# Performance work log

Hardware: AMD Instinct MI355X
Metric: run time of the kernel (lower is better)

Reference implementation:

```python
import jax, jax.numpy as jnp
import numpy as np

# Dimensions (all layers are mLSTM due to the constructor bug: `if w` tests the
# whole truthy `which` list, so signature=(2,1) still yields 3 mLSTM layers).
L, S, B, I = 3, 512, 4, 512      # layers, seq_len, batch, inp_dim
H, D = 8, 64                     # head_num, head_dim
HD = H * D                       # hidden dim = 512
P = 2 * I                        # up_l projection dim (m-branch p_factor = 2)
K = 4                            # causal conv kernel size
EPS = 1e-5
PNAMES = ['ln_g', 'ln_b', 'upl_w', 'upl_b', 'upr_w', 'upr_b', 'conv_w', 'conv_b',
          'wq_w', 'wq_b', 'wk_w', 'wk_b', 'wv_w', 'wv_b', 'wo_w', 'wo_b',
          'wi_w', 'wi_b', 'wf_w', 'wf_b', 'skip_w', 'gn_g', 'gn_b', 'down_w', 'down_b']


def setup_inputs() -> dict:
    key = jax.random.key(0)
    ks = iter(jax.random.split(key, 16))
    def w(shape, fan_in):
        return jax.random.normal(next(ks), shape, jnp.float32) / np.float32(np.sqrt(fan_in))
    return {
        'seq': jax.random.normal(next(ks), (S, B, I), jnp.float32),
        'ln_g': jnp.ones((L, I), jnp.float32), 'ln_b': jnp.zeros((L, I), jnp.float32),
        'upl_w': w((L, P, I), I), 'upl_b': jnp.zeros((L, P), jnp.float32),
        'upr_w': w((L, HD, I), I), 'upr_b': jnp.zeros((L, HD), jnp.float32),
        'conv_w': w((L, K), K), 'conv_b': jnp.zeros((L,), jnp.float32),
        'wq_w': w((L, HD, P), P), 'wq_b': jnp.zeros((L, HD), jnp.float32),
        'wk_w': w((L, HD, P), P), 'wk_b': jnp.zeros((L, HD), jnp.float32),
        'wv_w': w((L, HD, P), P), 'wv_b': jnp.zeros((L, HD), jnp.float32),
        'wo_w': w((L, HD, P), P), 'wo_b': jnp.zeros((L, HD), jnp.float32),
        'wi_w': w((L, H, P), P), 'wi_b': jnp.zeros((L, H), jnp.float32),
        'wf_w': w((L, H, P), P), 'wf_b': jnp.zeros((L, H), jnp.float32),
        'skip_w': w((L, HD, P), P),
        'gn_g': jnp.ones((L, HD), jnp.float32), 'gn_b': jnp.zeros((L, HD), jnp.float32),
        'down_w': w((L, I, HD), HD), 'down_b': jnp.zeros((L, I), jnp.float32),
    }


def _layernorm(x, g, b):
    mu = x.mean(-1, keepdims=True)
    v = ((x - mu) ** 2).mean(-1, keepdims=True)
    return (x - mu) / jnp.sqrt(v + EPS) * g + b


def _groupnorm(x, g, b):
    # GroupNorm(head_num, HD) on (B, HD): normalize each head's D channels
    xh = x.reshape(-1, H, D)
    mu = xh.mean(-1, keepdims=True)
    v = ((xh - mu) ** 2).mean(-1, keepdims=True)
    xn = (xh - mu) / jnp.sqrt(v + EPS)
    return (xn * g.reshape(H, D) + b.reshape(H, D)).reshape(-1, HD)


def _causal_conv(x, w, b):
    # 1-channel causal conv over the feature axis of the per-step vector (B, P)
    xp = jnp.pad(x, ((0, 0), (K - 1, 0)))
    y = b
    for k in range(K):  # K=4, static unroll
        y = y + w[k] * xp[:, k:k + x.shape[1]]
    return y


def _mlstm_step(p, x, state):
    c_, n_, m_ = state
    x_n = _layernorm(x, p['ln_g'], p['ln_b'])
    x_t = x_n @ p['upl_w'].T + p['upl_b']                 # (B, P)
    r_t = x_n @ p['upr_w'].T + p['upr_b']                 # (B, HD)
    x_c = jax.nn.silu(_causal_conv(x_t, p['conv_w'], p['conv_b']))
    q = (x_c @ p['wq_w'].T + p['wq_b']).reshape(-1, H, D)
    k = (x_c @ p['wk_w'].T + p['wk_b']).reshape(-1, H, D) / np.float32(np.sqrt(D))
    v = (x_t @ p['wv_w'].T + p['wv_b']).reshape(-1, H, D)
    i = x_c @ p['wi_w'].T + p['wi_b']                     # (B, H)
    f = x_c @ p['wf_w'].T + p['wf_b']                     # (B, H)
    o = jax.nn.sigmoid(x_t @ p['wo_w'].T + p['wo_b'])     # (B, HD)
    m = jnp.maximum(f + m_, i)                            # stabilizer
    ig = jnp.exp(i - m)
    fg = jnp.exp(f - m + m_)
    c = fg[..., None, None] * c_ + ig[..., None, None] * jnp.einsum('bhd,bhe->bhde', v, k)
    n = fg[..., None] * n_ + ig[..., None] * k
    num = jnp.einsum('bhde,bhe->bhd', c, q)
    den = jnp.maximum(jnp.abs(jnp.einsum('bhd,bhd->bh', n, q)), 1.0)[..., None]
    h = o * (num / den).reshape(-1, HD)
    out = _groupnorm(h, p['gn_g'], p['gn_b']) + x_c @ p['skip_w'].T
    out = out * jax.nn.silu(r_t)
    out = out @ p['down_w'].T + p['down_b']
    return out + x, (c, n, m)


def _forward(seq, params):
    b = seq.shape[1]
    def step(states, x_t):
        new_states = []
        inp = x_t
        for l in range(L):
            pl = {k: v[l] for k, v in params.items()}
            inp, st = _mlstm_step(pl, inp, states[l])
            new_states.append(st)
        return tuple(new_states), inp
    init = tuple((jnp.zeros((b, H, D, D), seq.dtype),
                  jnp.ones((b, H, D), seq.dtype),
                  jnp.zeros((b, H), seq.dtype)) for _ in range(L))
    _, out = jax.lax.scan(step, init, seq)
    return out  # (S, B, I)


def reference(seq, ln_g, ln_b, upl_w, upl_b, upr_w, upr_b, conv_w, conv_b,
              wq_w, wq_b, wk_w, wk_b, wv_w, wv_b, wo_w, wo_b,
              wi_w, wi_b, wf_w, wf_b, skip_w, gn_g, gn_b, down_w, down_b):
    params = dict(zip(PNAMES, [ln_g, ln_b, upl_w, upl_b, upr_w, upr_b, conv_w, conv_b,
                               wq_w, wq_b, wk_w, wk_b, wv_w, wv_b, wo_w, wo_b,
                               wi_w, wi_b, wf_w, wf_b, skip_w, gn_g, gn_b, down_w, down_b]))
    return _forward(seq, params)
```

## Files before the change

kernel.cpp:

```cpp
#include <hip/hip_runtime.h>
#include <hip/hip_bf16.h>
#include <cstdint>
#include <cstddef>

typedef short short8 __attribute__((ext_vector_type(8)));
typedef short short4v __attribute__((ext_vector_type(4)));
typedef float f32x4 __attribute__((ext_vector_type(4)));
typedef __hip_bfloat16 bf16;

#define NROW 2048
#define N1 1536
#define N2 1664
#define N3 1024
#define EPSV 1e-5f

static __device__ __forceinline__ bf16 f2bf(float v){ return __float2bfloat16(v); }
static __device__ __forceinline__ float bfbits2f(short s){
  unsigned u = ((unsigned)(unsigned short)s) << 16;
  float f; __builtin_memcpy(&f, &u, 4); return f;
}
static __device__ __forceinline__ void split_bf(float v, bf16& h, bf16& l){
  h = __float2bfloat16(v);
  l = __float2bfloat16(v - __bfloat162float(h));
}

static __device__ __forceinline__ void gload16(const bf16* g, bf16* l){
  __builtin_amdgcn_global_load_lds(
      (const __attribute__((address_space(1))) void*)(g),
      (__attribute__((address_space(3))) void*)(l), 16, 0, 0);
}

#define MFMA __builtin_amdgcn_mfma_f32_16x16x32_bf16

__global__ __launch_bounds__(256) void pack_w1(const float* __restrict__ upl,
    const float* __restrict__ upr, bf16* __restrict__ dh, bf16* __restrict__ dl)
{
  int l = blockIdx.y, r = blockIdx.x;
  const float* src = (r < 1024) ? upl + ((size_t)l*1024 + r)*512
                                : upr + ((size_t)l*512 + (r-1024))*512;
  size_t o = ((size_t)l*N1 + r)*512;
  for (int c = threadIdx.x; c < 512; c += 256) split_bf(src[c], dh[o+c], dl[o+c]);
}

__global__ __launch_bounds__(256) void pack_w2(const float* __restrict__ wq,
    const float* __restrict__ wk, const float* __restrict__ skp,
    const float* __restrict__ wi, const float* __restrict__ wf,
    bf16* __restrict__ dh, bf16* __restrict__ dl)
{
  int l = blockIdx.y, r = blockIdx.x;
  const float* src; float sc = 1.f;
  if (r < 512)        src = wq  + ((size_t)l*512 + r)*1024;
  else if (r < 1024){ src = wk  + ((size_t)l*512 + r-512)*1024; sc = 0.125f; }
  else if (r < 1536)  src = skp + ((size_t)l*512 + r-1024)*1024;
  else if (r < 1544)  src = wi  + ((size_t)l*8   + r-1536)*1024;
  else if (r < 1552)  src = wf  + ((size_t)l*8   + r-1544)*1024;
  else src = nullptr;
  size_t o = ((size_t)l*N2 + r)*1024;
  for (int c = threadIdx.x; c < 1024; c += 256)
    split_bf(src ? src[c]*sc : 0.f, dh[o+c], dl[o+c]);
}

__global__ __launch_bounds__(256) void pack_w3(const float* __restrict__ wv,
    const float* __restrict__ wo, bf16* __restrict__ dh, bf16* __restrict__ dl)
{
  int l = blockIdx.y, r = blockIdx.x;
  const float* src = (r < 512) ? wv + ((size_t)l*512 + r)*1024
                               : wo + ((size_t)l*512 + (r-512))*1024;
  size_t o = ((size_t)l*N3 + r)*1024;
  for (int c = threadIdx.x; c < 1024; c += 256) split_bf(src[c], dh[o+c], dl[o+c]);
}

__global__ __launch_bounds__(256) void pack_w4(const float* __restrict__ dw,
    bf16* __restrict__ dh, bf16* __restrict__ dl)
{
  int l = blockIdx.y, r = blockIdx.x;
  const float* src = dw + ((size_t)l*512 + r)*512;
  size_t o = ((size_t)l*512 + r)*512;
  for (int c = threadIdx.x; c < 512; c += 256) split_bf(src[c], dh[o+c], dl[o+c]);
}

__global__ __launch_bounds__(256) void pack_bias(
    const float* __restrict__ uplb, const float* __restrict__ uprb,
    const float* __restrict__ wqb,  const float* __restrict__ wkb,
    const float* __restrict__ wib,  const float* __restrict__ wfb,
    const float* __restrict__ wvb,  const float* __restrict__ wob,
    const float* __restrict__ dwb,
    float* __restrict__ b1, float* __restrict__ b2,
    float* __restrict__ b3, float* __restrict__ b4)
{
  int l = blockIdx.x;
  for (int j = threadIdx.x; j < N1; j += 256)
    b1[l*N1+j] = (j < 1024) ? uplb[l*1024+j] : uprb[l*512+j-1024];
  for (int j = threadIdx.x; j < N2; j += 256){
    float v = 0.f;
    if (j < 512)        v = wqb[l*512+j];
    else if (j < 1024)  v = wkb[l*512+j-512]*0.125f;
    else if (j < 1536)  v = 0.f;
    else if (j < 1544)  v = wib[l*8+j-1536];
    else if (j < 1552)  v = wfb[l*8+j-1544];
    b2[l*N2+j] = v;
  }
  for (int j = threadIdx.x; j < N3; j += 256)
    b3[l*N3+j] = (j < 512) ? wvb[l*512+j] : wob[l*512+j-512];
  for (int j = threadIdx.x; j < 512; j += 256)
    b4[l*512+j] = dwb[l*512+j];
}

static __device__ __forceinline__ void gemm_core(
    bf16* __restrict__ sm,
    int bx, int by,
    const bf16* __restrict__ Ah, const bf16* __restrict__ Al,
    const bf16* __restrict__ Wh, const bf16* __restrict__ Wl,
    const float* __restrict__ bias, float* __restrict__ Cf,
    bf16* __restrict__ Cbh, bf16* __restrict__ Cbl,
    const float* __restrict__ resid, int N, int K)
{
  int tid = threadIdx.x;
  int lane = tid & 63, w = tid >> 6;
  int wr = w >> 2, wc = w & 3;
  int m0 = by*128, n0 = bx*128;
  int srow = tid >> 2, sslot = tid & 3;
  int gcol = ((sslot ^ (srow & 3)) * 8);
  const bf16* gAh = Ah + (size_t)(m0 + srow)*K + gcol;
  const bf16* gAl = Al + (size_t)(m0 + srow)*K + gcol;
  const bf16* gBh = Wh + (size_t)(n0 + srow)*K + gcol;
  const bf16* gBl = Wl + (size_t)(n0 + srow)*K + gcol;

  f32x4 acc[4][2];
  for (int i=0;i<4;i++) for (int j=0;j<2;j++) acc[i][j] = (f32x4){0.f,0.f,0.f,0.f};

  int r = lane & 15, g = lane >> 4;
  int xs = (g ^ (r & 3)) * 8;
  int aoff[4], boff[2];
  for (int mi=0;mi<4;mi++) aoff[mi] = (wr*64 + mi*16 + r)*32 + xs;
  for (int ni=0;ni<2;ni++) boff[ni] = (wc*32 + ni*16 + r)*32 + xs;

  int nt = K >> 5;
#define STAGE_T(base, kk) do{ bf16* _d = sm + (base) + tid*8; \
    gload16(gAh + (kk), _d); \
    gload16(gAl + (kk), _d + 4096); \
    gload16(gBh + (kk), _d + 8192); \
    gload16(gBl + (kk), _d + 12288); }while(0)

  STAGE_T(0, 0);
  asm volatile("s_waitcnt vmcnt(0)" ::: "memory");
  __builtin_amdgcn_s_barrier();

  for (int t = 0; t < nt; ++t){
    int cb = (t & 1) * 16384;
    if (t + 1 < nt) STAGE_T(16384 - cb, (t+1)*32);
    const bf16* sA = sm + cb;
    short8 ah[4], al[4], bh2[2], bl2[2];
    for (int mi=0;mi<4;mi++){
      ah[mi] = *(const short8*)(sA + aoff[mi]);
      al[mi] = *(const short8*)(sA + 4096 + aoff[mi]);
    }
    for (int ni=0;ni<2;ni++){
      bh2[ni] = *(const short8*)(sA + 8192 + boff[ni]);
      bl2[ni] = *(const short8*)(sA + 12288 + boff[ni]);
    }
    for (int mi=0;mi<4;mi++) for (int ni=0;ni<2;ni++)
      acc[mi][ni] = MFMA(ah[mi], bh2[ni], acc[mi][ni],0,0,0);
    for (int mi=0;mi<4;mi++) for (int ni=0;ni<2;ni++)
      acc[mi][ni] = MFMA(al[mi], bh2[ni], acc[mi][ni],0,0,0);
    for (int mi=0;mi<4;mi++) for (int ni=0;ni<2;ni++)
      acc[mi][ni] = MFMA(ah[mi], bl2[ni], acc[mi][ni],0,0,0);
    asm volatile("s_waitcnt vmcnt(0)" ::: "memory");
    __builtin_amdgcn_s_barrier();
  }
#undef STAGE_T

  for (int mi=0;mi<4;mi++) for (int ni=0;ni<2;ni++){
    int col = n0 + wc*32 + ni*16 + r;
    float bv = bias ? bias[col] : 0.f;
    for (int j=0;j<4;j++){
      int row = m0 + wr*64 + mi*16 + g*4 + j;
      float v = acc[mi][ni][j] + bv;
      size_t o = (size_t)row*N + col;
      if (resid) v += resid[o];
      if (Cf) Cf[o] = v;
      if (Cbh) split_bf(v, Cbh[o], Cbl[o]);
    }
  }
}

__global__ __launch_bounds__(512) void gemm_std(
    const bf16* __restrict__ Ah, const bf16* __restrict__ Al,
    const bf16* __restrict__ Wh, const bf16* __restrict__ Wl,
    const float* __restrict__ bias, float* __restrict__ Cf,
    bf16* __restrict__ Cbh, bf16* __restrict__ Cbl,
    const float* __restrict__ resid, int N, int K, int nbx)
{
  __shared__ bf16 sm[2*4*4096];
  int id = blockIdx.x;
  int cpx = gridDim.x >> 3;
  int swz = (id & 7)*cpx + (id >> 3);
  int by = swz / nbx, bx = swz - by*nbx;
  gemm_core(sm, bx, by, Ah, Al, Wh, Wl, bias, Cf, Cbh, Cbl, resid, N, K);
}

__global__ __launch_bounds__(512) void gemm23(
    const bf16* __restrict__ A2h, const bf16* __restrict__ A2l,
    const bf16* __restrict__ W2h, const bf16* __restrict__ W2l,
    const float* __restrict__ b2,
    bf16* __restrict__ c2h, bf16* __restrict__ c2l,
    const bf16* __restrict__ A3h, const bf16* __restrict__ A3l,
    const bf16* __restrict__ W3h, const bf16* __restrict__ W3l,
    const float* __restrict__ b3,
    bf16* __restrict__ c3h, bf16* __restrict__ c3l)
{
  __shared__ bf16 sm[2*4*4096];
  int id = blockIdx.x;
  int cpx = gridDim.x >> 3;
  int swz = (id & 7)*cpx + (id >> 3);
  int by = swz / 21, bx = swz - by*21;
  if (bx < 13)
    gemm_core(sm, bx, by, A2h, A2l, W2h, W2l, b2, nullptr, c2h, c2l, nullptr, N2, 1024);
  else
    gemm_core(sm, bx-13, by, A3h, A3l, W3h, W3l, b3, nullptr, c3h, c3l, nullptr, N3, 1024);
}

__global__ __launch_bounds__(256) void ln_kernel(const float* __restrict__ x,
    const float* __restrict__ g, const float* __restrict__ bt,
    bf16* __restrict__ xnh, bf16* __restrict__ xnl)
{
  int row = blockIdx.x, t = threadIdx.x;
  float v0 = x[(size_t)row*512 + t], v1 = x[(size_t)row*512 + 256 + t];
  float s = v0 + v1, ss = v0*v0 + v1*v1;
  for (int m=1; m<64; m<<=1){ s += __shfl_xor(s,m); ss += __shfl_xor(ss,m); }
  __shared__ float sh[8];
  int w = t >> 6, lane = t & 63;
  if (lane == 0){ sh[w] = s; sh[4+w] = ss; }
  __syncthreads();
  s = sh[0]+sh[1]+sh[2]+sh[3]; ss = sh[4]+sh[5]+sh[6]+sh[7];
  float mu = s*(1.f/512.f), var = ss*(1.f/512.f) - mu*mu;
  float rs = rsqrtf(var + EPSV);
  float y0 = (v0-mu)*rs*g[t]     + bt[t];
  float y1 = (v1-mu)*rs*g[256+t] + bt[256+t];
  split_bf(y0, xnh[(size_t)row*512 + t],       xnl[(size_t)row*512 + t]);
  split_bf(y1, xnh[(size_t)row*512 + 256 + t], xnl[(size_t)row*512 + 256 + t]);
}

__global__ __launch_bounds__(256) void conv_kernel(
    const bf16* __restrict__ c1h, const bf16* __restrict__ c1l,
    const float* __restrict__ cw, const float* __restrict__ cb,
    bf16* __restrict__ xch, bf16* __restrict__ xcl,
    bf16* __restrict__ xth, bf16* __restrict__ xtl)
{
  int row = blockIdx.x;
  size_t rb = (size_t)row*N1;
  float w0=cw[0], w1=cw[1], w2=cw[2], w3=cw[3], bb=cb[0];
  int j0 = threadIdx.x*4;
  float x[7];
  for (int k=0;k<3;k++){
    int j = j0-3+k;
    x[k] = (j>=0) ? (bfbits2f(*(const short*)(c1h+rb+j)) +
                     bfbits2f(*(const short*)(c1l+rb+j))) : 0.f;
  }
  short4v h4 = *(const short4v*)(c1h+rb+j0);
  short4v l4 = *(const short4v*)(c1l+rb+j0);
  for (int k=0;k<4;k++) x[3+k] = bfbits2f(h4[k]) + bfbits2f(l4[k]);
  for (int i=0;i<4;i++){
    float y = bb + w0*x[i] + w1*x[i+1] + w2*x[i+2] + w3*x[i+3];
    float sg = 1.f/(1.f + __expf(-y));
    size_t o = (size_t)row*1024 + j0 + i;
    split_bf(y*sg, xch[o], xcl[o]);
    split_bf(x[3+i], xth[o], xtl[o]);
  }
}

__global__ __launch_bounds__(512) void scan_kernel(
    const bf16* __restrict__ c2h, const bf16* __restrict__ c2l,
    float* __restrict__ rowterm, float* __restrict__ colterm,
    float* __restrict__ den0)
{
  int bh = blockIdx.x, b = bh >> 3, h = bh & 7;
  int t = threadIdx.x;
  size_t rowoff = (size_t)(t*4+b)*N2;
  float fv = bfbits2f(*(const short*)(c2h+rowoff+1544+h)) +
             bfbits2f(*(const short*)(c2l+rowoff+1544+h));
  float iv = bfbits2f(*(const short*)(c2h+rowoff+1536+h)) +
             bfbits2f(*(const short*)(c2l+rowoff+1536+h));
  __shared__ double a[512];
  a[t] = (double)fv; __syncthreads();
  for (int off=1; off<512; off<<=1){
    double x = a[t];
    double y = (t >= off) ? a[t-off] : 0.0;
    __syncthreads();
    a[t] = x + y;
    __syncthreads();
  }
  float ct = (float)((double)iv - a[t]);
  colterm[bh*512 + t] = ct;
  __shared__ float mx[512];
  mx[t] = ct; __syncthreads();
  for (int off=1; off<512; off<<=1){
    float x = mx[t];
    float y = (t >= off) ? mx[t-off] : -3.0e38f;
    __syncthreads();
    mx[t] = fmaxf(x, y);
    __syncthreads();
  }
  float rt = -fmaxf(0.f, mx[t]);
  rowterm[bh*512 + t] = rt;
  float qs = 0.f;
  size_t qoff = rowoff + h*64;
  for (int c8=0;c8<8;c8++){
    short8 hx = *(const short8*)(c2h+qoff+c8*8);
    short8 lx = *(const short8*)(c2l+qoff+c8*8);
    for (int e=0;e<8;e++) qs += bfbits2f(hx[e]) + bfbits2f(lx[e]);
  }
  den0[bh*512 + t] = __expf(rt) * qs;
}

__global__ __launch_bounds__(512) void vtrans_kernel(
    const bf16* __restrict__ c3h, const bf16* __restrict__ c3l,
    bf16* __restrict__ vTh, bf16* __restrict__ vTl)
{
  int bh = blockIdx.y, b = bh >> 3, h = bh & 7;
  int d0 = blockIdx.x*8;
  int s = threadIdx.x;
  for (int dd=0; dd<8; dd++){
    int d = d0 + dd;
    size_t i = (size_t)(s*4+b)*N3 + h*64 + d;
    size_t o = ((size_t)bh*64 + d)*512 + s;
    vTh[o] = c3h[i];
    vTl[o] = c3l[i];
  }
}

__global__ __launch_bounds__(256) void attn_kernel(
    const bf16* __restrict__ c2h, const bf16* __restrict__ c2l,
    const bf16* __restrict__ vTh, const bf16* __restrict__ vTl,
    const float* __restrict__ rowt, const float* __restrict__ colt,
    float* __restrict__ num, float* __restrict__ denp)
{
  __shared__ bf16 Ph[32*64], Pl[32*64];
  int lane = threadIdx.x & 63, w = threadIdx.x >> 6;
  int tb = blockIdx.x, bh = blockIdx.y, b = bh >> 3, h = bh & 7;
  int t0 = tb*32;
  int r = lane & 15, g = lane >> 4;
  int rq = g*4;

  short8 qh[2][2], ql[2][2];
  for (int mi=0;mi<2;mi++) for (int k0=0;k0<2;k0++){
    size_t off = (size_t)((t0+mi*16+r)*4+b)*N2 + h*64 + k0*32 + g*8;
    qh[mi][k0] = *(const short8*)(c2h+off);
    ql[mi][k0] = *(const short8*)(c2l+off);
  }
  const float* rt = rowt + bh*512;
  const float* ctm = colt + bh*512;
  float rtv[2][4];
  for (int mi=0;mi<2;mi++) for (int j=0;j<4;j++) rtv[mi][j] = rt[t0+mi*16+rq+j];

  f32x4 accPV[2];
  for (int i=0;i<2;i++) accPV[i] = (f32x4){0.f,0.f,0.f,0.f};
  float rsum[2][4];
  for (int i=0;i<2;i++) for (int j=0;j<4;j++) rsum[i][j] = 0.f;

  int nsb = (tb >> 1) + 1;
  for (int sb=0; sb<nsb; ++sb){
    int s0 = sb*64;
    f32x4 acc[2];
    for (int i=0;i<2;i++) acc[i] = (f32x4){0.f,0.f,0.f,0.f};
    short8 kh[2], kl[2];
    for (int k0=0;k0<2;k0++){
      size_t off = (size_t)((s0+w*16+r)*4+b)*N2 + 512 + h*64 + k0*32 + g*8;
      kh[k0] = *(const short8*)(c2h+off);
      kl[k0] = *(const short8*)(c2l+off);
    }
    for (int k0=0;k0<2;k0++){
      for (int mi=0;mi<2;mi++) acc[mi] = MFMA(qh[mi][k0], kh[k0], acc[mi],0,0,0);
      for (int mi=0;mi<2;mi++) acc[mi] = MFMA(ql[mi][k0], kh[k0], acc[mi],0,0,0);
      for (int mi=0;mi<2;mi++) acc[mi] = MFMA(qh[mi][k0], kl[k0], acc[mi],0,0,0);
    }
    int sl = w*16 + r;
    int s = s0 + sl;
    float ctv = ctm[s];
    for (int mi=0;mi<2;mi++){
      for (int j=0;j<4;j++){
        int tloc = mi*16 + rq + j;
        int t = t0 + tloc;
        float wg = (s <= t) ? __expf(rtv[mi][j] + ctv) : 0.f;
        float gv = acc[mi][j] * wg;
        rsum[mi][j] += gv;
        int col = ((((sl>>3) ^ (tloc&7))<<3) | (sl&7));
        split_bf(gv, Ph[tloc*64+col], Pl[tloc*64+col]);
      }
    }
    __syncthreads();
    short8 vh[2], vl[2];
    for (int k0=0;k0<2;k0++){
      size_t off = ((size_t)bh*64 + w*16 + r)*512 + s0 + k0*32 + g*8;
      vh[k0] = *(const short8*)(vTh+off);
      vl[k0] = *(const short8*)(vTl+off);
    }
    for (int k0=0;k0<2;k0++){
      short8 ph[2], pl[2];
      for (int mi=0;mi<2;mi++){
        int tloc = mi*16 + r;
        int slot = (k0*4 + g) ^ (tloc&7);
        ph[mi] = *(const short8*)(&Ph[tloc*64 + slot*8]);
        pl[mi] = *(const short8*)(&Pl[tloc*64 + slot*8]);
      }
      for (int mi=0;mi<2;mi++) accPV[mi] = MFMA(ph[mi], vh[k0], accPV[mi],0,0,0);
      for (int mi=0;mi<2;mi++) accPV[mi] = MFMA(pl[mi], vh[k0], accPV[mi],0,0,0);
      for (int mi=0;mi<2;mi++) accPV[mi] = MFMA(ph[mi], vl[k0], accPV[mi],0,0,0);
    }
    __syncthreads();
  }

  for (int mi=0;mi<2;mi++)
    for (int j=0;j<4;j++){
      int t = t0 + mi*16 + rq + j;
      num[((size_t)bh*512 + t)*64 + w*16 + r] = accPV[mi][j];
    }
  for (int mi=0;mi<2;mi++)
    for (int j=0;j<4;j++){
      float v = rsum[mi][j];
      v += __shfl_xor(v,1); v += __shfl_xor(v,2);
      v += __shfl_xor(v,4); v += __shfl_xor(v,8);
      if (r == 0){
        int t = t0 + mi*16 + rq + j;
        denp[((size_t)bh*512 + t)*4 + w] = v;
      }
    }
}

__global__ __launch_bounds__(512) void h_kernel(
    const float* __restrict__ num, const float* __restrict__ den0,
    const float* __restrict__ denp,
    const bf16* __restrict__ c2h, const bf16* __restrict__ c2l,
    const bf16* __restrict__ c3h, const bf16* __restrict__ c3l,
    const bf16* __restrict__ c1h, const bf16* __restrict__ c1l,
    const float* __restrict__ gng, const float* __restrict__ gnb,
    bf16* __restrict__ oph, bf16* __restrict__ opl)
{
  int row = blockIdx.x, t = row >> 2, b = row & 3;
  int h = threadIdx.x >> 6, d = threadIdx.x & 63;
  int bh = b*8 + h;
  size_t bt = (size_t)bh*512 + t;
  float dn = den0[bt];
  for (int p=0; p<4; p++) dn += denp[bt*4 + p];
  dn = fmaxf(fabsf(dn), 1.f);
  float nv = num[bt*64 + d];
  size_t io = (size_t)row*N3 + 512 + h*64 + d;
  float ov = bfbits2f(*(const short*)(c3h+io)) + bfbits2f(*(const short*)(c3l+io));
  float o = 1.f/(1.f + __expf(-ov));
  float hv = o * nv / dn;
  float s = hv, ss = hv*hv;
  for (int m=1; m<64; m<<=1){ s += __shfl_xor(s,m); ss += __shfl_xor(ss,m); }
  float mu = s*(1.f/64.f), var = ss*(1.f/64.f) - mu*mu;
  float gn = (hv - mu)*rsqrtf(var + EPSV)*gng[h*64+d] + gnb[h*64+d];
  size_t ks = (size_t)row*N2 + 1024 + h*64 + d;
  float sk = bfbits2f(*(const short*)(c2h+ks)) + bfbits2f(*(const short*)(c2l+ks));
  size_t kr = (size_t)row*N1 + 1024 + h*64 + d;
  float rv = bfbits2f(*(const short*)(c1h+kr)) + bfbits2f(*(const short*)(c1l+kr));
  float y = (gn + sk) * (rv/(1.f + __expf(-rv)));
  size_t oo = (size_t)row*512 + h*64 + d;
  split_bf(y, oph[oo], opl[oo]);
}

extern "C" void kernel_launch(void* const* d_in, const int* in_sizes, int n_in,
                              void* d_out, int out_size, void* d_ws, size_t ws_size,
                              hipStream_t stream)
{
  (void)in_sizes; (void)n_in; (void)out_size; (void)ws_size;
  const float* seq    = (const float*)d_in[0];
  const float* ln_g   = (const float*)d_in[1];
  const float* ln_b   = (const float*)d_in[2];
  const float* upl_w  = (const float*)d_in[3];
  const float* upl_b  = (const float*)d_in[4];
  const float* upr_w  = (const float*)d_in[5];
  const float* upr_b  = (const float*)d_in[6];
  const float* conv_w = (const float*)d_in[7];
  const float* conv_b = (const float*)d_in[8];
  const float* wq_w   = (const float*)d_in[9];
  const float* wq_b   = (const float*)d_in[10];
  const float* wk_w   = (const float*)d_in[11];
  const float* wk_b   = (const float*)d_in[12];
  const float* wv_w   = (const float*)d_in[13];
  const float* wv_b   = (const float*)d_in[14];
  const float* wo_w   = (const float*)d_in[15];
  const float* wo_b   = (const float*)d_in[16];
  const float* wi_w   = (const float*)d_in[17];
  const float* wi_b   = (const float*)d_in[18];
  const float* wf_w   = (const float*)d_in[19];
  const float* wf_b   = (const float*)d_in[20];
  const float* skip_w = (const float*)d_in[21];
  const float* gn_g   = (const float*)d_in[22];
  const float* gn_b   = (const float*)d_in[23];
  const float* down_w = (const float*)d_in[24];
  const float* down_b = (const float*)d_in[25];

  char* ws = (char*)d_ws;
  size_t off = 0;
  auto alloc = [&](size_t bytes)->char*{
    char* p = ws + off; off = (off + bytes + 255) & ~(size_t)255; return p;
  };
  bf16*  W1h = (bf16*)alloc((size_t)3*N1*512*2);
  bf16*  W1l = (bf16*)alloc((size_t)3*N1*512*2);
  bf16*  W2h = (bf16*)alloc((size_t)3*N2*1024*2);
  bf16*  W2l = (bf16*)alloc((size_t)3*N2*1024*2);
  bf16*  W3h = (bf16*)alloc((size_t)3*N3*1024*2);
  bf16*  W3l = (bf16*)alloc((size_t)3*N3*1024*2);
  bf16*  W4h = (bf16*)alloc((size_t)3*512*512*2);
  bf16*  W4l = (bf16*)alloc((size_t)3*512*512*2);
  float* b1  = (float*)alloc((size_t)3*N1*4);
  float* b2  = (float*)alloc((size_t)3*N2*4);
  float* b3  = (float*)alloc((size_t)3*N3*4);
  float* b4  = (float*)alloc((size_t)3*512*4);
  bf16*  xnh = (bf16*)alloc((size_t)NROW*512*2);
  bf16*  xnl = (bf16*)alloc((size_t)NROW*512*2);
  bf16*  c1h = (bf16*)alloc((size_t)NROW*N1*2);
  bf16*  c1l = (bf16*)alloc((size_t)NROW*N1*2);
  bf16*  xth = (bf16*)alloc((size_t)NROW*1024*2);
  bf16*  xtl = (bf16*)alloc((size_t)NROW*1024*2);
  bf16*  xch = (bf16*)alloc((size_t)NROW*1024*2);
  bf16*  xcl = (bf16*)alloc((size_t)NROW*1024*2);
  bf16*  c2h = (bf16*)alloc((size_t)NROW*N2*2);
  bf16*  c2l = (bf16*)alloc((size_t)NROW*N2*2);
  bf16*  c3h = (bf16*)alloc((size_t)NROW*N3*2);
  bf16*  c3l = (bf16*)alloc((size_t)NROW*N3*2);
  bf16*  vTh = (bf16*)alloc((size_t)32*64*512*2);
  bf16*  vTl = (bf16*)alloc((size_t)32*64*512*2);
  float* rowt= (float*)alloc((size_t)32*512*4);
  float* colt= (float*)alloc((size_t)32*512*4);
  float* den0= (float*)alloc((size_t)32*512*4);
  float* denp= (float*)alloc((size_t)32*512*4*4);
  float* num = (float*)alloc((size_t)32*512*64*4);
  bf16*  oph = (bf16*)alloc((size_t)NROW*512*2);
  bf16*  opl = (bf16*)alloc((size_t)NROW*512*2);
  float* xA  = (float*)alloc((size_t)NROW*512*4);
  float* xB  = (float*)alloc((size_t)NROW*512*4);

  pack_w1<<<dim3(N1,3), 256, 0, stream>>>(upl_w, upr_w, W1h, W1l);
  pack_w2<<<dim3(N2,3), 256, 0, stream>>>(wq_w, wk_w, skip_w, wi_w, wf_w, W2h, W2l);
  pack_w3<<<dim3(N3,3), 256, 0, stream>>>(wv_w, wo_w, W3h, W3l);
  pack_w4<<<dim3(512,3), 256, 0, stream>>>(down_w, W4h, W4l);
  pack_bias<<<3, 256, 0, stream>>>(upl_b, upr_b, wq_b, wk_b, wi_b, wf_b,
                                   wv_b, wo_b, down_b, b1, b2, b3, b4);

  for (int l = 0; l < 3; l++){
    const float* x_in = (l == 0) ? seq : ((l == 1) ? xA : xB);
    float* x_out = (l == 0) ? xA : ((l == 1) ? xB : (float*)d_out);

    ln_kernel<<<NROW, 256, 0, stream>>>(x_in, ln_g + l*512, ln_b + l*512, xnh, xnl);
    gemm_std<<<12*16, 512, 0, stream>>>(
        xnh, xnl, W1h + (size_t)l*N1*512, W1l + (size_t)l*N1*512,
        b1 + l*N1, nullptr, c1h, c1l, nullptr, N1, 512, 12);
    conv_kernel<<<NROW, 256, 0, stream>>>(c1h, c1l, conv_w + l*4, conv_b + l,
                                          xch, xcl, xth, xtl);
    gemm23<<<21*16, 512, 0, stream>>>(
        xch, xcl, W2h + (size_t)l*N2*1024, W2l + (size_t)l*N2*1024, b2 + l*N2,
        c2h, c2l,
        xth, xtl, W3h + (size_t)l*N3*1024, W3l + (size_t)l*N3*1024, b3 + l*N3,
        c3h, c3l);
    scan_kernel<<<32, 512, 0, stream>>>(c2h, c2l, rowt, colt, den0);
    vtrans_kernel<<<dim3(8,32), 512, 0, stream>>>(c3h, c3l, vTh, vTl);
    attn_kernel<<<dim3(16,32), 256, 0, stream>>>(c2h, c2l, vTh, vTl,
                                                 rowt, colt, num, denp);
    h_kernel<<<NROW, 512, 0, stream>>>(num, den0, denp, c2h, c2l, c3h, c3l,
                                       c1h, c1l, gn_g + l*512, gn_b + l*512,
                                       oph, opl);
    gemm_std<<<4*16, 512, 0, stream>>>(
        oph, opl, W4h + (size_t)l*512*512, W4l + (size_t)l*512*512,
        b4 + l*512, x_out, nullptr, nullptr, x_in, 512, 512, 4);
  }
}
```

Before: 459.8 us.

## Merge pack and prep kernels, use 64-row GEMM tiles, warp-level scans

Merges the four weight-pack kernels and the bias pack into one launch, and merges the gate scan with the V transpose into a single prep kernel. The scan now runs in one wavefront using register prefix sums and shuffles instead of a 512-thread LDS scan with many barriers. The q-sum denominator term moves into h_kernel. The up-projection and down-projection GEMMs switch to a 64x128-tile, 256-thread variant so more blocks fill the device. The aim is to cut launch count, barrier latency and under-occupancy of the small GEMMs, at the cost of less weight reuse per tile.

Measured after the change: 410.0 us. 10.8% less time.

```diff
diff --git a/kernel.cpp b/kernel.cpp
--- a/kernel.cpp
+++ b/kernel.cpp
@@ -32,78 +32,72 @@
 
 #define MFMA __builtin_amdgcn_mfma_f32_16x16x32_bf16
 
-__global__ __launch_bounds__(256) void pack_w1(const float* __restrict__ upl,
-    const float* __restrict__ upr, bf16* __restrict__ dh, bf16* __restrict__ dl)
-{
-  int l = blockIdx.y, r = blockIdx.x;
-  const float* src = (r < 1024) ? upl + ((size_t)l*1024 + r)*512
-                                : upr + ((size_t)l*512 + (r-1024))*512;
-  size_t o = ((size_t)l*N1 + r)*512;
-  for (int c = threadIdx.x; c < 512; c += 256) split_bf(src[c], dh[o+c], dl[o+c]);
-}
-
-__global__ __launch_bounds__(256) void pack_w2(const float* __restrict__ wq,
-    const float* __restrict__ wk, const float* __restrict__ skp,
-    const float* __restrict__ wi, const float* __restrict__ wf,
-    bf16* __restrict__ dh, bf16* __restrict__ dl)
-{
-  int l = blockIdx.y, r = blockIdx.x;
-  const float* src; float sc = 1.f;
-  if (r < 512)        src = wq  + ((size_t)l*512 + r)*1024;
-  else if (r < 1024){ src = wk  + ((size_t)l*512 + r-512)*1024; sc = 0.125f; }
-  else if (r < 1536)  src = skp + ((size_t)l*512 + r-1024)*1024;
-  else if (r < 1544)  src = wi  + ((size_t)l*8   + r-1536)*1024;
-  else if (r < 1552)  src = wf  + ((size_t)l*8   + r-1544)*1024;
-  else src = nullptr;
-  size_t o = ((size_t)l*N2 + r)*1024;
-  for (int c = threadIdx.x; c < 1024; c += 256)
-    split_bf(src ? src[c]*sc : 0.f, dh[o+c], dl[o+c]);
-}
-
-__global__ __launch_bounds__(256) void pack_w3(const float* __restrict__ wv,
-    const float* __restrict__ wo, bf16* __restrict__ dh, bf16* __restrict__ dl)
-{
-  int l = blockIdx.y, r = blockIdx.x;
-  const float* src = (r < 512) ? wv + ((size_t)l*512 + r)*1024
-                               : wo + ((size_t)l*512 + (r-512))*1024;
-  size_t o = ((size_t)l*N3 + r)*1024;
-  for (int c = threadIdx.x; c < 1024; c += 256) split_bf(src[c], dh[o+c], dl[o+c]);
-}
-
-__global__ __launch_bounds__(256) void pack_w4(const float* __restrict__ dw,
-    bf16* __restrict__ dh, bf16* __restrict__ dl)
-{
-  int l = blockIdx.y, r = blockIdx.x;
-  const float* src = dw + ((size_t)l*512 + r)*512;
-  size_t o = ((size_t)l*512 + r)*512;
-  for (int c = threadIdx.x; c < 512; c += 256) split_bf(src[c], dh[o+c], dl[o+c]);
-}
-
-__global__ __launch_bounds__(256) void pack_bias(
+__global__ __launch_bounds__(256) void pack_all(
+    const float* __restrict__ upl, const float* __restrict__ upr,
+    const float* __restrict__ wq,  const float* __restrict__ wk,
+    const float* __restrict__ skp, const float* __restrict__ wi,
+    const float* __restrict__ wf,  const float* __restrict__ wv,
+    const float* __restrict__ wo,  const float* __restrict__ dw,
     const float* __restrict__ uplb, const float* __restrict__ uprb,
     const float* __restrict__ wqb,  const float* __restrict__ wkb,
     const float* __restrict__ wib,  const float* __restrict__ wfb,
     const float* __restrict__ wvb,  const float* __restrict__ wob,
     const float* __restrict__ dwb,
+    bf16* __restrict__ W1h, bf16* __restrict__ W1l,
+    bf16* __restrict__ W2h, bf16* __restrict__ W2l,
+    bf16* __restrict__ W3h, bf16* __restrict__ W3l,
+    bf16* __restrict__ W4h, bf16* __restrict__ W4l,
     float* __restrict__ b1, float* __restrict__ b2,
     float* __restrict__ b3, float* __restrict__ b4)
 {
-  int l = blockIdx.x;
-  for (int j = threadIdx.x; j < N1; j += 256)
-    b1[l*N1+j] = (j < 1024) ? uplb[l*1024+j] : uprb[l*512+j-1024];
-  for (int j = threadIdx.x; j < N2; j += 256){
-    float v = 0.f;
-    if (j < 512)        v = wqb[l*512+j];
-    else if (j < 1024)  v = wkb[l*512+j-512]*0.125f;
-    else if (j < 1536)  v = 0.f;
-    else if (j < 1544)  v = wib[l*8+j-1536];
-    else if (j < 1552)  v = wfb[l*8+j-1544];
-    b2[l*N2+j] = v;
-  }
-  for (int j = threadIdx.x; j < N3; j += 256)
-    b3[l*N3+j] = (j < 512) ? wvb[l*512+j] : wob[l*512+j-512];
-  for (int j = threadIdx.x; j < 512; j += 256)
-    b4[l*512+j] = dwb[l*512+j];
+  int l = blockIdx.y;
+  int bx = blockIdx.x;
+  if (bx < 1536){
+    int r = bx;
+    const float* src = (r < 1024) ? upl + ((size_t)l*1024 + r)*512
+                                  : upr + ((size_t)l*512 + (r-1024))*512;
+    size_t o = ((size_t)l*N1 + r)*512;
+    for (int c = threadIdx.x; c < 512; c += 256) split_bf(src[c], W1h[o+c], W1l[o+c]);
+  } else if (bx < 3200){
+    int r = bx - 1536;
+    const float* src; float sc = 1.f;
+    if (r < 512)        src = wq  + ((size_t)l*512 + r)*1024;
+    else if (r < 1024){ src = wk  + ((size_t)l*512 + r-512)*1024; sc = 0.125f; }
+    else if (r < 1536)  src = skp + ((size_t)l*512 + r-1024)*1024;
+    else if (r < 1544)  src = wi  + ((size_t)l*8   + r-1536)*1024;
+    else if (r < 1552)  src = wf  + ((size_t)l*8   + r-1544)*1024;
+    else src = nullptr;
+    size_t o = ((size_t)l*N2 + r)*1024;
+    for (int c = threadIdx.x; c < 1024; c += 256)
+      split_bf(src ? src[c]*sc : 0.f, W2h[o+c], W2l[o+c]);
+  } else if (bx < 4224){
+    int r = bx - 3200;
+    const float* src = (r < 512) ? wv + ((size_t)l*512 + r)*1024
+                                 : wo + ((size_t)l*512 + (r-512))*1024;
+    size_t o = ((size_t)l*N3 + r)*1024;
+    for (int c = threadIdx.x; c < 1024; c += 256) split_bf(src[c], W3h[o+c], W3l[o+c]);
+  } else if (bx < 4736){
+    int r = bx - 4224;
+    const float* src = dw + ((size_t)l*512 + r)*512;
+    size_t o = ((size_t)l*512 + r)*512;
+    for (int c = threadIdx.x; c < 512; c += 256) split_bf(src[c], W4h[o+c], W4l[o+c]);
+  } else {
+    for (int j = threadIdx.x; j < N1; j += 256)
+      b1[l*N1+j] = (j < 1024) ? uplb[l*1024+j] : uprb[l*512+j-1024];
+    for (int j = threadIdx.x; j < N2; j += 256){
+      float v = 0.f;
+      if (j < 512)        v = wqb[l*512+j];
+      else if (j < 1024)  v = wkb[l*512+j-512]*0.125f;
+      else if (j < 1536)  v = 0.f;
+      else if (j < 1544)  v = wib[l*8+j-1536];
+      else if (j < 1552)  v = wfb[l*8+j-1544];
+      b2[l*N2+j] = v;
+    }
+    for (int j = threadIdx.x; j < N3; j += 256)
+      b3[l*N3+j] = (j < 512) ? wvb[l*512+j] : wob[l*512+j-512];
+    for (int j = threadIdx.x; j < 512; j += 256)
+      b4[l*512+j] = dwb[l*512+j];
+  }
 }
 
 static __device__ __forceinline__ void gemm_core(
@@ -184,6 +178,84 @@
   }
 }
 
+static __device__ __forceinline__ void gemm_core64(
+    bf16* __restrict__ sm,
+    int bx, int by,
+    const bf16* __restrict__ Ah, const bf16* __restrict__ Al,
+    const bf16* __restrict__ Wh, const bf16* __restrict__ Wl,
+    const float* __restrict__ bias, float* __restrict__ Cf,
+    bf16* __restrict__ Cbh, bf16* __restrict__ Cbl,
+    const float* __restrict__ resid, int N, int K)
+{
+  int tid = threadIdx.x;
+  int lane = tid & 63, w = tid >> 6;
+  int m0 = by*64, n0 = bx*128;
+  int srow = tid >> 2, sslot = tid & 3;
+  int gcol = ((sslot ^ (srow & 3)) * 8);
+  const bf16* gAh = Ah + (size_t)(m0 + srow)*K + gcol;
+  const bf16* gAl = Al + (size_t)(m0 + srow)*K + gcol;
+  const bf16* gBh = Wh + (size_t)(n0 + srow)*K + gcol;
+  const bf16* gBl = Wl + (size_t)(n0 + srow)*K + gcol;
+  size_t pstr = (size_t)64*K;
+
+  f32x4 acc[4][2];
+  for (int i=0;i<4;i++) for (int j=0;j<2;j++) acc[i][j] = (f32x4){0.f,0.f,0.f,0.f};
+
+  int r = lane & 15, g = lane >> 4;
+  int xs = (g ^ (r & 3)) * 8;
+  int aoff[4], boff[2];
+  for (int mi=0;mi<4;mi++) aoff[mi] = (mi*16 + r)*32 + xs;
+  for (int ni=0;ni<2;ni++) boff[ni] = (w*32 + ni*16 + r)*32 + xs;
+
+  int nt = K >> 5;
+#define STAGE64(base, kk) do{ bf16* _d = sm + (base) + tid*8; \
+    gload16(gAh + (kk), _d); \
+    gload16(gAl + (kk), _d + 2048); \
+    gload16(gBh + (kk), _d + 4096);  gload16(gBh + (kk) + pstr, _d + 6144); \
+    gload16(gBl + (kk), _d + 8192);  gload16(gBl + (kk) + pstr, _d + 10240); }while(0)
+
+  STAGE64(0, 0);
+  asm volatile("s_waitcnt vmcnt(0)" ::: "memory");
+  __builtin_amdgcn_s_barrier();
+
+  for (int t = 0; t < nt; ++t){
+    int cb = (t & 1) * 12288;
+    if (t + 1 < nt) STAGE64(12288 - cb, (t+1)*32);
+    const bf16* sA = sm + cb;
+    short8 ah[4], al[4], bh2[2], bl2[2];
+    for (int mi=0;mi<4;mi++){
+      ah[mi] = *(const short8*)(sA + aoff[mi]);
+      al[mi] = *(const short8*)(sA + 2048 + aoff[mi]);
+    }
+    for (int ni=0;ni<2;ni++){
+      bh2[ni] = *(const short8*)(sA + 4096 + boff[ni]);
+      bl2[ni] = *(const short8*)(sA + 8192 + boff[ni]);
+    }
+    for (int mi=0;mi<4;mi++) for (int ni=0;ni<2;ni++)
+      acc[mi][ni] = MFMA(ah[mi], bh2[ni], acc[mi][ni],0,0,0);
+    for (int mi=0;mi<4;mi++) for (int ni=0;ni<2;ni++)
+      acc[mi][ni] = MFMA(al[mi], bh2[ni], acc[mi][ni],0,0,0);
+    for (int mi=0;mi<4;mi++) for (int ni=0;ni<2;ni++)
+      acc[mi][ni] = MFMA(ah[mi], bl2[ni], acc[mi][ni],0,0,0);
+    asm volatile("s_waitcnt vmcnt(0)" ::: "memory");
+    __builtin_amdgcn_s_barrier();
+  }
+#undef STAGE64
+
+  for (int mi=0;mi<4;mi++) for (int ni=0;ni<2;ni++){
+    int col = n0 + w*32 + ni*16 + r;
+    float bv = bias ? bias[col] : 0.f;
+    for (int j=0;j<4;j++){
+      int row = m0 + mi*16 + g*4 + j;
+      float v = acc[mi][ni][j] + bv;
+      size_t o = (size_t)row*N + col;
+      if (resid) v += resid[o];
+      if (Cf) Cf[o] = v;
+      if (Cbh) split_bf(v, Cbh[o], Cbl[o]);
+    }
+  }
+}
+
 __global__ __launch_bounds__(512) void gemm_std(
     const bf16* __restrict__ Ah, const bf16* __restrict__ Al,
     const bf16* __restrict__ Wh, const bf16* __restrict__ Wl,
@@ -197,6 +269,21 @@
   int swz = (id & 7)*cpx + (id >> 3);
   int by = swz / nbx, bx = swz - by*nbx;
   gemm_core(sm, bx, by, Ah, Al, Wh, Wl, bias, Cf, Cbh, Cbl, resid, N, K);
+}
+
+__global__ __launch_bounds__(256) void gemm_s64(
+    const bf16* __restrict__ Ah, const bf16* __restrict__ Al,
+    const bf16* __restrict__ Wh, const bf16* __restrict__ Wl,
+    const float* __restrict__ bias, float* __restrict__ Cf,
+    bf16* __restrict__ Cbh, bf16* __restrict__ Cbl,
+    const float* __restrict__ resid, int N, int K, int nbx)
+{
+  __shared__ bf16 sm[2*12288];
+  int id = blockIdx.x;
+  int cpx = gridDim.x >> 3;
+  int swz = (id & 7)*cpx + (id >> 3);
+  int by = swz / nbx, bx = swz - by*nbx;
+  gemm_core64(sm, bx, by, Ah, Al, Wh, Wl, bias, Cf, Cbh, Cbl, resid, N, K);
 }
 
 __global__ __launch_bounds__(512) void gemm23(
@@ -269,63 +356,61 @@
   }
 }
 
-__global__ __launch_bounds__(512) void scan_kernel(
+__global__ __launch_bounds__(512) void prep_kernel(
+    const bf16* __restrict__ c3h, const bf16* __restrict__ c3l,
     const bf16* __restrict__ c2h, const bf16* __restrict__ c2l,
-    float* __restrict__ rowterm, float* __restrict__ colterm,
-    float* __restrict__ den0)
-{
-  int bh = blockIdx.x, b = bh >> 3, h = bh & 7;
-  int t = threadIdx.x;
-  size_t rowoff = (size_t)(t*4+b)*N2;
-  float fv = bfbits2f(*(const short*)(c2h+rowoff+1544+h)) +
-             bfbits2f(*(const short*)(c2l+rowoff+1544+h));
-  float iv = bfbits2f(*(const short*)(c2h+rowoff+1536+h)) +
-             bfbits2f(*(const short*)(c2l+rowoff+1536+h));
-  __shared__ double a[512];
-  a[t] = (double)fv; __syncthreads();
-  for (int off=1; off<512; off<<=1){
-    double x = a[t];
-    double y = (t >= off) ? a[t-off] : 0.0;
-    __syncthreads();
-    a[t] = x + y;
-    __syncthreads();
-  }
-  float ct = (float)((double)iv - a[t]);
-  colterm[bh*512 + t] = ct;
-  __shared__ float mx[512];
-  mx[t] = ct; __syncthreads();
-  for (int off=1; off<512; off<<=1){
-    float x = mx[t];
-    float y = (t >= off) ? mx[t-off] : -3.0e38f;
-    __syncthreads();
-    mx[t] = fmaxf(x, y);
-    __syncthreads();
-  }
-  float rt = -fmaxf(0.f, mx[t]);
-  rowterm[bh*512 + t] = rt;
-  float qs = 0.f;
-  size_t qoff = rowoff + h*64;
-  for (int c8=0;c8<8;c8++){
-    short8 hx = *(const short8*)(c2h+qoff+c8*8);
-    short8 lx = *(const short8*)(c2l+qoff+c8*8);
-    for (int e=0;e<8;e++) qs += bfbits2f(hx[e]) + bfbits2f(lx[e]);
-  }
-  den0[bh*512 + t] = __expf(rt) * qs;
-}
-
-__global__ __launch_bounds__(512) void vtrans_kernel(
-    const bf16* __restrict__ c3h, const bf16* __restrict__ c3l,
-    bf16* __restrict__ vTh, bf16* __restrict__ vTl)
+    bf16* __restrict__ vTh, bf16* __restrict__ vTl,
+    float* __restrict__ rowterm, float* __restrict__ colterm)
 {
   int bh = blockIdx.y, b = bh >> 3, h = bh & 7;
-  int d0 = blockIdx.x*8;
-  int s = threadIdx.x;
-  for (int dd=0; dd<8; dd++){
-    int d = d0 + dd;
-    size_t i = (size_t)(s*4+b)*N3 + h*64 + d;
-    size_t o = ((size_t)bh*64 + d)*512 + s;
-    vTh[o] = c3h[i];
-    vTl[o] = c3l[i];
+  if (blockIdx.x < 8){
+    int d0 = blockIdx.x*8;
+    int s = threadIdx.x;
+    for (int dd=0; dd<8; dd++){
+      int d = d0 + dd;
+      size_t i = (size_t)(s*4+b)*N3 + h*64 + d;
+      size_t o = ((size_t)bh*64 + d)*512 + s;
+      vTh[o] = c3h[i];
+      vTl[o] = c3l[i];
+    }
+    return;
+  }
+  if (threadIdx.x >= 64) return;
+  int lane = threadIdx.x;
+  double fv[8]; float iv[8];
+  for (int j=0;j<8;j++){
+    int t = lane*8 + j;
+    size_t ro = (size_t)(t*4+b)*N2;
+    fv[j] = (double)(bfbits2f(*(const short*)(c2h+ro+1544+h)) +
+                     bfbits2f(*(const short*)(c2l+ro+1544+h)));
+    iv[j] = bfbits2f(*(const short*)(c2h+ro+1536+h)) +
+            bfbits2f(*(const short*)(c2l+ro+1536+h));
+  }
+  double ps[8]; double s = 0.0;
+  for (int j=0;j<8;j++){ s += fv[j]; ps[j] = s; }
+  double run = s;
+  for (int o=1;o<64;o<<=1){
+    double u = __shfl_up(run, o);
+    if (lane >= o) run += u;
+  }
+  double excl = run - s;
+  float ct[8];
+  for (int j=0;j<8;j++){
+    ct[j] = (float)((double)iv[j] - (excl + ps[j]));
+    colterm[bh*512 + lane*8 + j] = ct[j];
+  }
+  float pm[8]; float mm = -3.0e38f;
+  for (int j=0;j<8;j++){ mm = fmaxf(mm, ct[j]); pm[j] = mm; }
+  float incl = mm;
+  for (int o=1;o<64;o<<=1){
+    float u = __shfl_up(incl, o);
+    if (lane >= o) incl = fmaxf(incl, u);
+  }
+  float ex = __shfl_up(incl, 1);
+  if (lane == 0) ex = -3.0e38f;
+  for (int j=0;j<8;j++){
+    float inc = fmaxf(ex, pm[j]);
+    rowterm[bh*512 + lane*8 + j] = -fmaxf(0.f, inc);
   }
 }
 
@@ -428,8 +513,8 @@
 }
 
 __global__ __launch_bounds__(512) void h_kernel(
-    const float* __restrict__ num, const float* __restrict__ den0,
-    const float* __restrict__ denp,
+    const float* __restrict__ num, const float* __restrict__ denp,
+    const float* __restrict__ rowt,
     const bf16* __restrict__ c2h, const bf16* __restrict__ c2l,
     const bf16* __restrict__ c3h, const bf16* __restrict__ c3l,
     const bf16* __restrict__ c1h, const bf16* __restrict__ c1l,
@@ -440,7 +525,10 @@
   int h = threadIdx.x >> 6, d = threadIdx.x & 63;
   int bh = b*8 + h;
   size_t bt = (size_t)bh*512 + t;
-  float dn = den0[bt];
+  size_t qo = (size_t)row*N2 + h*64 + d;
+  float qs = bfbits2f(*(const short*)(c2h+qo)) + bfbits2f(*(const short*)(c2l+qo));
+  for (int m=1; m<64; m<<=1) qs += __shfl_xor(qs, m);
+  float dn = __expf(rowt[bt]) * qs;
   for (int p=0; p<4; p++) dn += denp[bt*4 + p];
   dn = fmaxf(fabsf(dn), 1.f);
   float nv = num[bt*64 + d];
@@ -526,7 +614,6 @@
   bf16*  vTl = (bf16*)alloc((size_t)32*64*512*2);
   float* rowt= (float*)alloc((size_t)32*512*4);
   float* colt= (float*)alloc((size_t)32*512*4);
-  float* den0= (float*)alloc((size_t)32*512*4);
   float* denp= (float*)alloc((size_t)32*512*4*4);
   float* num = (float*)alloc((size_t)32*512*64*4);
   bf16*  oph = (bf16*)alloc((size_t)NROW*512*2);
@@ -534,19 +621,17 @@
   float* xA  = (float*)alloc((size_t)NROW*512*4);
   float* xB  = (float*)alloc((size_t)NROW*512*4);
 
-  pack_w1<<<dim3(N1,3), 256, 0, stream>>>(upl_w, upr_w, W1h, W1l);
-  pack_w2<<<dim3(N2,3), 256, 0, stream>>>(wq_w, wk_w, skip_w, wi_w, wf_w, W2h, W2l);
-  pack_w3<<<dim3(N3,3), 256, 0, stream>>>(wv_w, wo_w, W3h, W3l);
-  pack_w4<<<dim3(512,3), 256, 0, stream>>>(down_w, W4h, W4l);
-  pack_bias<<<3, 256, 0, stream>>>(upl_b, upr_b, wq_b, wk_b, wi_b, wf_b,
-                                   wv_b, wo_b, down_b, b1, b2, b3, b4);
+  pack_all<<<dim3(4737,3), 256, 0, stream>>>(
+      upl_w, upr_w, wq_w, wk_w, skip_w, wi_w, wf_w, wv_w, wo_w, down_w,
+      upl_b, upr_b, wq_b, wk_b, wi_b, wf_b, wv_b, wo_b, down_b,
+      W1h, W1l, W2h, W2l, W3h, W3l, W4h, W4l, b1, b2, b3, b4);
 
   for (int l = 0; l < 3; l++){
     const float* x_in = (l == 0) ? seq : ((l == 1) ? xA : xB);
     float* x_out = (l == 0) ? xA : ((l == 1) ? xB : (float*)d_out);
 
     ln_kernel<<<NROW, 256, 0, stream>>>(x_in, ln_g + l*512, ln_b + l*512, xnh, xnl);
-    gemm_std<<<12*16, 512, 0, stream>>>(
+    gemm_s64<<<32*12, 256, 0, stream>>>(
         xnh, xnl, W1h + (size_t)l*N1*512, W1l + (size_t)l*N1*512,
         b1 + l*N1, nullptr, c1h, c1l, nullptr, N1, 512, 12);
     conv_kernel<<<NROW, 256, 0, stream>>>(c1h, c1l, conv_w + l*4, conv_b + l,
@@ -556,14 +641,14 @@
         c2h, c2l,
         xth, xtl, W3h + (size_t)l*N3*1024, W3l + (size_t)l*N3*1024, b3 + l*N3,
         c3h, c3l);
-    scan_kernel<<<32, 512, 0, stream>>>(c2h, c2l, rowt, colt, den0);
-    vtrans_kernel<<<dim3(8,32), 512, 0, stream>>>(c3h, c3l, vTh, vTl);
+    prep_kernel<<<dim3(9,32), 512, 0, stream>>>(c3h, c3l, c2h, c2l,
+                                                vTh, vTl, rowt, colt);
     attn_kernel<<<dim3(16,32), 256, 0, stream>>>(c2h, c2l, vTh, vTl,
                                                  rowt, colt, num, denp);
-    h_kernel<<<NROW, 512, 0, stream>>>(num, den0, denp, c2h, c2l, c3h, c3l,
+    h_kernel<<<NROW, 512, 0, stream>>>(num, denp, rowt, c2h, c2l, c3h, c3l,
                                        c1h, c1l, gn_g + l*512, gn_b + l*512,
                                        oph, opl);
-    gemm_std<<<4*16, 512, 0, stream>>>(
+    gemm_s64<<<32*4, 256, 0, stream>>>(
         oph, opl, W4h + (size_t)l*512*512, W4l + (size_t)l*512*512,
         b4 + l*512, x_out, nullptr, nullptr, x_in, 512, 512, 4);
   }
```
